# Optimization experiments

Measured on AMD Instinct MI355X. Metric: run time of the kernel, lower is better.

The kernel has to match this reference:

```python
import jax, jax.numpy as jnp
import numpy as np

DIM = 768
HEADS = 12
HEAD_DIM = DIM // HEADS
SCALE = HEAD_DIM ** -0.5
ALPHA = 0.1


def setup_inputs() -> dict:
    key = jax.random.key(0)
    ks = jax.random.split(key, 6)
    B, N, C = 16, 577, DIM
    x = jax.random.normal(ks[0], (B, N, C), dtype=jnp.float32)
    attn_weight = jax.random.uniform(ks[1], (B, N - 1), dtype=jnp.float32)
    w_qkv = jax.random.normal(ks[2], (C, 3 * C), dtype=jnp.float32) * (C ** -0.5)
    b_qkv = jnp.zeros((3 * C,), dtype=jnp.float32)
    w_proj = jax.random.normal(ks[3], (C, C), dtype=jnp.float32) * (C ** -0.5)
    b_proj = jnp.zeros((C,), dtype=jnp.float32)
    return {"x": x, "attn_weight": attn_weight, "w_qkv": w_qkv, "b_qkv": b_qkv,
            "w_proj": w_proj, "b_proj": b_proj}


def reference(x, attn_weight, w_qkv, b_qkv, w_proj, b_proj):
    B, N, C = x.shape
    H, D = HEADS, HEAD_DIM
    qkv = (x @ w_qkv + b_qkv).reshape(B, N, 3, H, D)
    qkv = jnp.transpose(qkv, (2, 0, 3, 1, 4))  # [3, B, H, N, D]
    q, k, v = qkv[0], qkv[1], qkv[2]
    attn = jnp.einsum('bhnd,bhmd->bhnm', q, k) * SCALE  # [B,H,N,N]
    patch_attn = attn[:, :, 0, 1:]  # pre-softmax CLS->patch scores
    # reweight CLS row (excluding CLS->CLS) before softmax
    w = attn_weight[:, None, None, :]  # [B,1,1,N-1]
    cls_row = attn[:, :, 0:1, 1:] * (w * ALPHA + (1.0 - ALPHA))
    attn = attn.at[:, :, 0:1, 1:].set(cls_row)
    attn = jax.nn.softmax(attn, axis=-1)
    out = jnp.einsum('bhnm,bhmd->bhnd', attn, v)
    out = jnp.transpose(out, (0, 2, 1, 3)).reshape(B, N, C)
    out = out @ w_proj + b_proj
    return out, patch_attn
```

## Files before the change

kernel.cpp:

```cpp
#include <hip/hip_runtime.h>
#include <hip/hip_bf16.h>
#include <math.h>

#define B_    16
#define N_    577
#define C_    768
#define H_    12
#define D_    64
#define M_    (B_ * N_)
#define MP_   9344
#define QKVN  2304
#define NP_   640
#define SCALE 0.125f
#define ALPHA 0.1f
#define OUT0  (B_ * N_ * C_)

#define NB_CONV 7008
#define NB_T1   1728
#define NB_T2   576

typedef __attribute__((ext_vector_type(8))) short short8;
typedef __attribute__((ext_vector_type(4))) float f32x4;
typedef __hip_bfloat16 bf16;

__device__ __forceinline__ float exp2fast(float x) {
    return __builtin_amdgcn_exp2f(x);
}

__device__ __forceinline__ void load16(const void* g, void* l) {
    __builtin_amdgcn_global_load_lds(
        (const __attribute__((address_space(1))) unsigned int*)g,
        (__attribute__((address_space(3))) unsigned int*)l, 16, 0, 0);
}

__device__ __forceinline__ f32x4 mfma16(short8 a, short8 b, f32x4 c) {
    return __builtin_amdgcn_mfma_f32_16x16x32_bf16(a, b, c, 0, 0, 0);
}

#define FENCE() asm volatile("" ::: "memory")
#define BARRIER() do { FENCE(); __builtin_amdgcn_s_barrier(); FENCE(); } while (0)

__global__ __launch_bounds__(256) void prep(const float* __restrict__ x,
                                            bf16* __restrict__ xb,
                                            const float* __restrict__ wq,
                                            bf16* __restrict__ wqT,
                                            const float* __restrict__ wp,
                                            bf16* __restrict__ wpT) {
    __shared__ float tile[32][33];
    const int bid = blockIdx.x;
    if (bid < NB_CONV) {
        int idx = bid * 256 + threadIdx.x;
        int m = idx / 192;
        bf16 tmp[4];
        if (m < M_) {
            float4 f = ((const float4*)x)[idx];
            tmp[0] = __float2bfloat16(f.x);
            tmp[1] = __float2bfloat16(f.y);
            tmp[2] = __float2bfloat16(f.z);
            tmp[3] = __float2bfloat16(f.w);
        } else {
            tmp[0] = tmp[1] = tmp[2] = tmp[3] = __float2bfloat16(0.f);
        }
        ((ushort4*)xb)[idx] = *(ushort4*)tmp;
        return;
    }
    const float* src; bf16* dst; int C, R, bx, by;
    if (bid < NB_CONV + NB_T1) {
        int r = bid - NB_CONV;
        bx = r % 72; by = r / 72; src = wq; dst = wqT; R = 768; C = QKVN;
    } else {
        int r = bid - NB_CONV - NB_T1;
        bx = r % 24; by = r / 24; src = wp; dst = wpT; R = 768; C = 768;
    }
    int cb = bx * 32, rb = by * 32;
    int tx = threadIdx.x & 31, ty = threadIdx.x >> 5;
    #pragma unroll
    for (int i = 0; i < 32; i += 8)
        tile[ty + i][tx] = src[(size_t)(rb + ty + i) * C + cb + tx];
    __syncthreads();
    #pragma unroll
    for (int i = 0; i < 32; i += 8)
        dst[(size_t)(cb + ty + i) * R + rb + tx] = __float2bfloat16(tile[tx][ty + i]);
}

__global__ __launch_bounds__(256, 4) void gemm128(const bf16* __restrict__ A,
                                                  const bf16* __restrict__ BT,
                                                  const float* __restrict__ bias,
                                                  bf16* __restrict__ q,
                                                  bf16* __restrict__ kk,
                                                  bf16* __restrict__ vt,
                                                  float* __restrict__ out,
                                                  int mode, int nby) {
    __shared__ __align__(16) char smem[35840];

    const int nwg = gridDim.x;
    const int orig = blockIdx.x;
    const int xcd = orig & 7, ii = orig >> 3;
    const int qq = nwg >> 3, rr = nwg & 7;
    const int wg = (xcd < rr ? xcd * (qq + 1) : rr * (qq + 1) + (xcd - rr) * qq) + ii;
    const int mb = wg / nby;
    const int nb = wg - mb * nby;
    const int m0 = mb * 128, n0 = nb * 128;
    const int t = threadIdx.x, lane = t & 63, w = t >> 6;
    const int wr = w >> 1, wc = w & 1;
    const int r16 = lane & 15, quad = lane >> 4;

    f32x4 acc[4][4];
    #pragma unroll
    for (int i = 0; i < 4; i++)
        #pragma unroll
        for (int j = 0; j < 4; j++) acc[i][j] = (f32x4)(0.f);

    const int lrow = lane >> 3;
    const int clog = ((lane & 7) ^ lrow) << 4;
    const char* gA = (const char*)A  + (size_t)(m0 + w * 32 + lrow) * 1536 + clog;
    const char* gB = (const char*)BT + (size_t)(n0 + w * 32 + lrow) * 1536 + clog;

    auto stage = [&](int k2) {
        const int kc = k2 * 128;
        #pragma unroll
        for (int i = 0; i < 4; i++) {
            char* dA = (char*)smem + w * 4096 + i * 1024;
            load16(gA + (size_t)i * 12288 + kc, dA);
            load16(gB + (size_t)i * 12288 + kc, dA + 16384);
        }
    };

    stage(0);
    asm volatile("s_waitcnt vmcnt(0)" ::: "memory");
    BARRIER();

    const int sw = r16 & 7;
    const int g0 = (quad ^ sw) << 4;
    const int g1 = ((quad ^ 4) ^ sw) << 4;

    #pragma unroll 1
    for (int k = 0; k < 12; k++) {
        const char* Ap = (const char*)smem + (wr * 64 + r16) * 128;
        const char* Bp = (const char*)smem + 16384 + (wc * 64 + r16) * 128;

        short8 a[4], b[4];
        #pragma unroll
        for (int mi = 0; mi < 4; mi++) a[mi] = *(const short8*)(Ap + mi * 2048 + g0);
        #pragma unroll
        for (int nj = 0; nj < 4; nj++) b[nj] = *(const short8*)(Bp + nj * 2048 + g0);
        __builtin_amdgcn_s_setprio(1);
        #pragma unroll
        for (int mi = 0; mi < 4; mi++)
            #pragma unroll
            for (int nj = 0; nj < 4; nj++)
                acc[mi][nj] = mfma16(a[mi], b[nj], acc[mi][nj]);
        __builtin_amdgcn_s_setprio(0);

        #pragma unroll
        for (int mi = 0; mi < 4; mi++) a[mi] = *(const short8*)(Ap + mi * 2048 + g1);
        #pragma unroll
        for (int nj = 0; nj < 4; nj++) b[nj] = *(const short8*)(Bp + nj * 2048 + g1);
        __builtin_amdgcn_s_setprio(1);
        #pragma unroll
        for (int mi = 0; mi < 4; mi++)
            #pragma unroll
            for (int nj = 0; nj < 4; nj++)
                acc[mi][nj] = mfma16(a[mi], b[nj], acc[mi][nj]);
        __builtin_amdgcn_s_setprio(0);

        BARRIER();
        if (k < 11) {
            stage(k + 1);
            asm volatile("s_waitcnt vmcnt(0)" ::: "memory");
            BARRIER();
        }
    }

    float bs[4];
    #pragma unroll
    for (int nj = 0; nj < 4; nj++) bs[nj] = bias[n0 + wc * 64 + nj * 16 + r16];

    if (mode == 1) {
        #pragma unroll
        for (int mi = 0; mi < 4; mi++) {
            #pragma unroll
            for (int nj = 0; nj < 4; nj++) {
                #pragma unroll
                for (int r = 0; r < 4; r++) {
                    int m = m0 + wr * 64 + mi * 16 + quad * 4 + r;
                    if (m >= M_) continue;
                    int cc = n0 + wc * 64 + nj * 16 + r16;
                    out[(size_t)m * 768 + cc] = acc[mi][nj][r] + bs[nj];
                }
            }
        }
        return;
    }

    bf16* Tt = (bf16*)smem;
    #pragma unroll
    for (int mi = 0; mi < 4; mi++) {
        #pragma unroll
        for (int nj = 0; nj < 4; nj++) {
            bf16 pk[4];
            #pragma unroll
            for (int r = 0; r < 4; r++)
                pk[r] = __float2bfloat16(acc[mi][nj][r] + bs[nj]);
            int ccl = wc * 64 + nj * 16 + r16;
            int ml4 = wr * 64 + mi * 16 + quad * 4;
            *(uint2*)&Tt[ccl * 140 + ml4] = *(const uint2*)pk;
        }
    }
    __syncthreads();

    const int part = nb / 6;
    if (part < 2) {
        int nl = t & 127, half = t >> 7;
        int m = m0 + nl;
        if (m < M_) {
            int b = m / N_, n = m - b * N_;
            int h = (nb % 6) * 2 + half;
            bf16* dst = (part == 0 ? q : kk) + ((size_t)(b * H_ + h) * N_ + n) * 64;
            #pragma unroll
            for (int d8 = 0; d8 < 8; d8++) {
                bf16 tv[8];
                #pragma unroll
                for (int dd = 0; dd < 8; dd++)
                    tv[dd] = Tt[(half * 64 + d8 * 8 + dd) * 140 + nl];
                *(uint4*)(dst + d8 * 8) = *(const uint4*)tv;
            }
        }
    } else {
        int dr = t >> 1, seg = t & 1;
        int rem = (nb % 6) * 128 + dr;
        int h = rem >> 6, d = rem & 63;
        int mb2 = m0 + seg * 64;
        int b = mb2 / N_;
        int n = mb2 - b * N_;
        const bf16* src = Tt + dr * 140 + seg * 64;
        int i = 0;
        while (i < 64 && mb2 + i < M_) {
            if (n == N_) { b++; n = 0; }
            bf16* drow = vt + ((size_t)(b * H_ + h) * 64 + d) * NP_;
            if ((n & 7) == 0 && n + 8 <= N_ && i + 8 <= 64 && mb2 + i + 8 <= M_) {
                bf16 tv[8];
                #pragma unroll
                for (int dd = 0; dd < 8; dd++) tv[dd] = src[i + dd];
                *(uint4*)(drow + n) = *(const uint4*)tv;
                i += 8; n += 8;
            } else {
                drow[n] = src[i]; i++; n++;
            }
        }
    }
}

__global__ __launch_bounds__(256) void attn_mfma(const bf16* __restrict__ q,
                                                 const bf16* __restrict__ k,
                                                 const bf16* __restrict__ vt,
                                                 const float* __restrict__ aw,
                                                 bf16* __restrict__ ao,
                                                 float* __restrict__ patch) {
    __shared__ bf16 Kb[2][4096];
    __shared__ bf16 Vb[2][4096];
    __shared__ bf16 Pb[4][2048];
    const int bh = blockIdx.x, qt = blockIdx.y;
    const int b = bh / H_, h = bh - b * H_;
    const int t = threadIdx.x, lane = t & 63, w = t >> 6;
    const int r16 = lane & 15, quad = lane >> 4;
    const float SC2 = SCALE * 1.44269504f;

    const bf16* kbp = k + (size_t)bh * N_ * 64;
    const bf16* vbp = vt + (size_t)bh * 64 * NP_;

    short8 qa0[2], qa1[2];
    #pragma unroll
    for (int mi = 0; mi < 2; mi++) {
        int qrow = qt * 128 + w * 32 + mi * 16 + r16;
        int qrc = (qrow < N_) ? qrow : (N_ - 1);
        const bf16* qp = q + ((size_t)bh * N_ + qrc) * 64 + quad * 8;
        qa0[mi] = *(const short8*)(qp);
        qa1[mi] = *(const short8*)(qp + 32);
    }

    f32x4 Oacc[2][4];
    #pragma unroll
    for (int mi = 0; mi < 2; mi++)
        #pragma unroll
        for (int d0 = 0; d0 < 4; d0++) Oacc[mi][d0] = (f32x4)(0.f);
    float lrow[2][4];
    #pragma unroll
    for (int mi = 0; mi < 2; mi++)
        #pragma unroll
        for (int rr = 0; rr < 4; rr++) lrow[mi][rr] = 0.f;

    const bool clsrow = (qt == 0) && (w == 0) && (quad == 0);

    auto stage = [&](int kt, int buf) {
        #pragma unroll
        for (int is = 0; is < 2; is++) {
            int base = is * 256 + w * 64;
            int slot = base + lane;
            int row = slot >> 3, pos = slot & 7;
            int c = pos ^ (row & 7);
            int jg = kt * 64 + row; if (jg > N_ - 1) jg = N_ - 1;
            load16(kbp + (size_t)jg * 64 + c * 8, &Kb[buf][base * 8]);
        }
        #pragma unroll
        for (int is = 0; is < 2; is++) {
            int base = is * 256 + w * 64;
            int slot = base + lane;
            int row = slot >> 3, pos = slot & 7;
            int c = pos ^ (row & 7);
            load16(vbp + (size_t)row * NP_ + kt * 64 + c * 8, &Vb[buf][base * 8]);
        }
    };

    stage(0, 0);
    __syncthreads();

    for (int kt = 0; kt < 10; kt++) {
        const int cur = kt & 1;
        if (kt < 9) stage(kt + 1, cur ^ 1);

        f32x4 S[2][4];
        #pragma unroll
        for (int j0 = 0; j0 < 4; j0++) {
            int row = j0 * 16 + r16;
            const bf16* kpl = &Kb[cur][row * 64];
            short8 kf0 = *(const short8*)(kpl + ((quad ^ (row & 7)) << 3));
            short8 kf1 = *(const short8*)(kpl + (((quad ^ 4) ^ (row & 7)) << 3));
            #pragma unroll
            for (int mi = 0; mi < 2; mi++) {
                f32x4 sa = (f32x4)(0.f);
                sa = mfma16(qa0[mi], kf0, sa);
                sa = mfma16(qa1[mi], kf1, sa);
                S[mi][j0] = sa;
            }
        }

        if (kt < 9) {
            #pragma unroll
            for (int mi = 0; mi < 2; mi++) {
                #pragma unroll
                for (int j0 = 0; j0 < 4; j0++) {
                    float wfac = 1.f;
                    if (mi == 0 && clsrow) {
                        int c = kt * 64 + j0 * 16 + r16;
                        if (c >= 1) {
                            patch[(size_t)bh * (N_ - 1) + (c - 1)] = S[0][j0][0] * SCALE;
                            wfac = aw[b * (N_ - 1) + (c - 1)] * ALPHA + (1.f - ALPHA);
                        }
                    }
                    #pragma unroll
                    for (int rr = 0; rr < 4; rr++) {
                        float v = S[mi][j0][rr] * SC2;
                        if (rr == 0) v *= wfac;
                        float p = exp2fast(v);
                        S[mi][j0][rr] = p;
                        lrow[mi][rr] += p;
                    }
                }
            }
        } else {
            #pragma unroll
            for (int mi = 0; mi < 2; mi++) {
                #pragma unroll
                for (int j0 = 0; j0 < 4; j0++) {
                    int c = kt * 64 + j0 * 16 + r16;
                    bool valid = (c < N_);
                    float wfac = 1.f;
                    if (mi == 0 && clsrow && valid) {
                        patch[(size_t)bh * (N_ - 1) + (c - 1)] = S[0][j0][0] * SCALE;
                        wfac = aw[b * (N_ - 1) + (c - 1)] * ALPHA + (1.f - ALPHA);
                    }
                    #pragma unroll
                    for (int rr = 0; rr < 4; rr++) {
                        float v = S[mi][j0][rr] * SC2;
                        if (rr == 0) v *= wfac;
                        float p = valid ? exp2fast(v) : 0.f;
                        S[mi][j0][rr] = p;
                        lrow[mi][rr] += p;
                    }
                }
            }
        }

        bf16* pw = &Pb[w][0];
        #pragma unroll
        for (int mi = 0; mi < 2; mi++) {
            #pragma unroll
            for (int j0 = 0; j0 < 4; j0++) {
                int cg = j0 * 2 + (r16 >> 3);
                #pragma unroll
                for (int rr = 0; rr < 4; rr++) {
                    int rp = mi * 16 + quad * 4 + rr;
                    pw[rp * 64 + ((cg ^ (rp & 7)) << 3) + (r16 & 7)] =
                        __float2bfloat16(S[mi][j0][rr]);
                }
            }
        }
        short8 pa0[2], pa1[2];
        #pragma unroll
        for (int mi = 0; mi < 2; mi++) {
            int rp = mi * 16 + r16;
            const bf16* pr = pw + rp * 64;
            pa0[mi] = *(const short8*)(pr + ((quad ^ (rp & 7)) << 3));
            pa1[mi] = *(const short8*)(pr + (((quad ^ 4) ^ (rp & 7)) << 3));
        }

        #pragma unroll
        for (int d0 = 0; d0 < 4; d0++) {
            int row = d0 * 16 + r16;
            const bf16* vpl = &Vb[cur][row * 64];
            short8 vf0 = *(const short8*)(vpl + ((quad ^ (row & 7)) << 3));
            short8 vf1 = *(const short8*)(vpl + (((quad ^ 4) ^ (row & 7)) << 3));
            #pragma unroll
            for (int mi = 0; mi < 2; mi++) {
                Oacc[mi][d0] = mfma16(pa0[mi], vf0, Oacc[mi][d0]);
                Oacc[mi][d0] = mfma16(pa1[mi], vf1, Oacc[mi][d0]);
            }
        }
        __syncthreads();
    }

    #pragma unroll
    for (int mi = 0; mi < 2; mi++) {
        #pragma unroll
        for (int rr = 0; rr < 4; rr++) {
            float l = lrow[mi][rr];
            l += __shfl_xor(l, 1);
            l += __shfl_xor(l, 2);
            l += __shfl_xor(l, 4);
            l += __shfl_xor(l, 8);
            int n = qt * 128 + w * 32 + mi * 16 + quad * 4 + rr;
            if (n >= N_) continue;
            float inv = 1.f / l;
            #pragma unroll
            for (int d0 = 0; d0 < 4; d0++) {
                ao[((size_t)(b * N_ + n) * H_ + h) * 64 + d0 * 16 + r16] =
                    __float2bfloat16(Oacc[mi][d0][rr] * inv);
            }
        }
    }
}

extern "C" void kernel_launch(void* const* d_in, const int* in_sizes, int n_in,
                              void* d_out, int out_size, void* d_ws, size_t ws_size,
                              hipStream_t stream) {
    const float* x      = (const float*)d_in[0];
    const float* aw     = (const float*)d_in[1];
    const float* w_qkv  = (const float*)d_in[2];
    const float* b_qkv  = (const float*)d_in[3];
    const float* w_proj = (const float*)d_in[4];
    const float* b_proj = (const float*)d_in[5];
    float* out = (float*)d_out;

    char* ws = (char*)d_ws;
    bf16* xbf    = (bf16*)(ws);
    bf16* wqkvT  = (bf16*)(ws + 14352384);
    bf16* wprojT = (bf16*)(ws + 17891328);
    bf16* qv     = (bf16*)(ws + 19070976);
    bf16* kv     = (bf16*)(ws + 33251328);
    bf16* vt     = (bf16*)(ws + 47431680);
    bf16* ao     = xbf;

    prep<<<NB_CONV + NB_T1 + NB_T2, 256, 0, stream>>>(x, xbf, w_qkv, wqkvT, w_proj, wprojT);

    gemm128<<<73 * 18, 256, 0, stream>>>(
        xbf, wqkvT, b_qkv, qv, kv, vt, nullptr, 0, 18);

    attn_mfma<<<dim3(H_ * B_, 5), 256, 0, stream>>>(qv, kv, vt, aw, ao, out + OUT0);

    gemm128<<<73 * 6, 256, 0, stream>>>(
        ao, wprojT, b_proj, nullptr, nullptr, nullptr, out, 1, 6);
}
```

Before: 216.8 us.

## Widen GEMM tiles to 128x256 with each wave owning a 64-column strip

The GEMM tile grows from 128x128 to 128x256. Each of the four waves now computes the full 128 rows against its own 64 columns, holding 8x4 accumulators, and the grid shrinks by half for both the QKV and projection launches. The goal is more reuse of each loaded A tile and fewer workgroups re-reading A from memory. The costs are higher register and LDS pressure (occupancy hint drops from 4 to 3) and fewer blocks: 219 for the projection GEMM, which may underfill 256 CUs. The scatter epilogue now runs in two phases because the LDS transpose buffer holds only 128 columns at a time.

```diff
diff --git a/kernel.cpp b/kernel.cpp
--- a/kernel.cpp
+++ b/kernel.cpp
@@ -83,15 +83,15 @@
         dst[(size_t)(cb + ty + i) * R + rb + tx] = __float2bfloat16(tile[tx][ty + i]);
 }
 
-__global__ __launch_bounds__(256, 4) void gemm128(const bf16* __restrict__ A,
-                                                  const bf16* __restrict__ BT,
-                                                  const float* __restrict__ bias,
-                                                  bf16* __restrict__ q,
-                                                  bf16* __restrict__ kk,
-                                                  bf16* __restrict__ vt,
-                                                  float* __restrict__ out,
-                                                  int mode, int nby) {
-    __shared__ __align__(16) char smem[35840];
+__global__ __launch_bounds__(256, 3) void gemmw(const bf16* __restrict__ A,
+                                                const bf16* __restrict__ BT,
+                                                const float* __restrict__ bias,
+                                                bf16* __restrict__ q,
+                                                bf16* __restrict__ kk,
+                                                bf16* __restrict__ vt,
+                                                float* __restrict__ out,
+                                                int mode, int nby) {
+    __shared__ __align__(16) char smem[49152];
 
     const int nwg = gridDim.x;
     const int orig = blockIdx.x;
@@ -100,29 +100,29 @@
     const int wg = (xcd < rr ? xcd * (qq + 1) : rr * (qq + 1) + (xcd - rr) * qq) + ii;
     const int mb = wg / nby;
     const int nb = wg - mb * nby;
-    const int m0 = mb * 128, n0 = nb * 128;
+    const int m0 = mb * 128, n0 = nb * 256;
     const int t = threadIdx.x, lane = t & 63, w = t >> 6;
-    const int wr = w >> 1, wc = w & 1;
     const int r16 = lane & 15, quad = lane >> 4;
 
-    f32x4 acc[4][4];
-    #pragma unroll
-    for (int i = 0; i < 4; i++)
+    f32x4 acc[8][4];
+    #pragma unroll
+    for (int i = 0; i < 8; i++)
         #pragma unroll
         for (int j = 0; j < 4; j++) acc[i][j] = (f32x4)(0.f);
 
     const int lrow = lane >> 3;
     const int clog = ((lane & 7) ^ lrow) << 4;
-    const char* gA = (const char*)A  + (size_t)(m0 + w * 32 + lrow) * 1536 + clog;
-    const char* gB = (const char*)BT + (size_t)(n0 + w * 32 + lrow) * 1536 + clog;
+    const char* gA = (const char*)A  + (size_t)(m0 + lrow) * 1536 + clog;
+    const char* gB = (const char*)BT + (size_t)(n0 + lrow) * 1536 + clog;
 
     auto stage = [&](int k2) {
         const int kc = k2 * 128;
         #pragma unroll
-        for (int i = 0; i < 4; i++) {
-            char* dA = (char*)smem + w * 4096 + i * 1024;
-            load16(gA + (size_t)i * 12288 + kc, dA);
-            load16(gB + (size_t)i * 12288 + kc, dA + 16384);
+        for (int i = 0; i < 12; i++) {
+            const int s = w * 12 + i;
+            const char* src = (s < 16) ? (gA + (size_t)s * 12288 + kc)
+                                       : (gB + (size_t)(s - 16) * 12288 + kc);
+            load16(src, (char*)smem + s * 1024);
         }
     };
 
@@ -134,34 +134,53 @@
     const int g0 = (quad ^ sw) << 4;
     const int g1 = ((quad ^ 4) ^ sw) << 4;
 
+    const char* Ap = (const char*)smem + r16 * 128;
+    const char* Bp = (const char*)smem + 16384 + (w * 64 + r16) * 128;
+
     #pragma unroll 1
     for (int k = 0; k < 12; k++) {
-        const char* Ap = (const char*)smem + (wr * 64 + r16) * 128;
-        const char* Bp = (const char*)smem + 16384 + (wc * 64 + r16) * 128;
-
-        short8 a[4], b[4];
-        #pragma unroll
-        for (int mi = 0; mi < 4; mi++) a[mi] = *(const short8*)(Ap + mi * 2048 + g0);
+        short8 a4[4], b[4];
+
         #pragma unroll
         for (int nj = 0; nj < 4; nj++) b[nj] = *(const short8*)(Bp + nj * 2048 + g0);
+        #pragma unroll
+        for (int mi = 0; mi < 4; mi++) a4[mi] = *(const short8*)(Ap + mi * 2048 + g0);
         __builtin_amdgcn_s_setprio(1);
         #pragma unroll
         for (int mi = 0; mi < 4; mi++)
             #pragma unroll
             for (int nj = 0; nj < 4; nj++)
-                acc[mi][nj] = mfma16(a[mi], b[nj], acc[mi][nj]);
+                acc[mi][nj] = mfma16(a4[mi], b[nj], acc[mi][nj]);
         __builtin_amdgcn_s_setprio(0);
-
-        #pragma unroll
-        for (int mi = 0; mi < 4; mi++) a[mi] = *(const short8*)(Ap + mi * 2048 + g1);
+        #pragma unroll
+        for (int mi = 0; mi < 4; mi++) a4[mi] = *(const short8*)(Ap + (mi + 4) * 2048 + g0);
+        __builtin_amdgcn_s_setprio(1);
+        #pragma unroll
+        for (int mi = 0; mi < 4; mi++)
+            #pragma unroll
+            for (int nj = 0; nj < 4; nj++)
+                acc[mi + 4][nj] = mfma16(a4[mi], b[nj], acc[mi + 4][nj]);
+        __builtin_amdgcn_s_setprio(0);
+
         #pragma unroll
         for (int nj = 0; nj < 4; nj++) b[nj] = *(const short8*)(Bp + nj * 2048 + g1);
+        #pragma unroll
+        for (int mi = 0; mi < 4; mi++) a4[mi] = *(const short8*)(Ap + mi * 2048 + g1);
         __builtin_amdgcn_s_setprio(1);
         #pragma unroll
         for (int mi = 0; mi < 4; mi++)
             #pragma unroll
             for (int nj = 0; nj < 4; nj++)
-                acc[mi][nj] = mfma16(a[mi], b[nj], acc[mi][nj]);
+                acc[mi][nj] = mfma16(a4[mi], b[nj], acc[mi][nj]);
+        __builtin_amdgcn_s_setprio(0);
+        #pragma unroll
+        for (int mi = 0; mi < 4; mi++) a4[mi] = *(const short8*)(Ap + (mi + 4) * 2048 + g1);
+        __builtin_amdgcn_s_setprio(1);
+        #pragma unroll
+        for (int mi = 0; mi < 4; mi++)
+            #pragma unroll
+            for (int nj = 0; nj < 4; nj++)
+                acc[mi + 4][nj] = mfma16(a4[mi], b[nj], acc[mi + 4][nj]);
         __builtin_amdgcn_s_setprio(0);
 
         BARRIER();
@@ -174,18 +193,18 @@
 
     float bs[4];
     #pragma unroll
-    for (int nj = 0; nj < 4; nj++) bs[nj] = bias[n0 + wc * 64 + nj * 16 + r16];
+    for (int nj = 0; nj < 4; nj++) bs[nj] = bias[n0 + w * 64 + nj * 16 + r16];
 
     if (mode == 1) {
         #pragma unroll
-        for (int mi = 0; mi < 4; mi++) {
+        for (int mi = 0; mi < 8; mi++) {
             #pragma unroll
             for (int nj = 0; nj < 4; nj++) {
                 #pragma unroll
                 for (int r = 0; r < 4; r++) {
-                    int m = m0 + wr * 64 + mi * 16 + quad * 4 + r;
+                    int m = m0 + mi * 16 + quad * 4 + r;
                     if (m >= M_) continue;
-                    int cc = n0 + wc * 64 + nj * 16 + r16;
+                    int cc = n0 + w * 64 + nj * 16 + r16;
                     out[(size_t)m * 768 + cc] = acc[mi][nj][r] + bs[nj];
                 }
             }
@@ -195,57 +214,63 @@
 
     bf16* Tt = (bf16*)smem;
     #pragma unroll
-    for (int mi = 0; mi < 4; mi++) {
-        #pragma unroll
-        for (int nj = 0; nj < 4; nj++) {
-            bf16 pk[4];
-            #pragma unroll
-            for (int r = 0; r < 4; r++)
-                pk[r] = __float2bfloat16(acc[mi][nj][r] + bs[nj]);
-            int ccl = wc * 64 + nj * 16 + r16;
-            int ml4 = wr * 64 + mi * 16 + quad * 4;
-            *(uint2*)&Tt[ccl * 140 + ml4] = *(const uint2*)pk;
-        }
-    }
-    __syncthreads();
-
-    const int part = nb / 6;
-    if (part < 2) {
-        int nl = t & 127, half = t >> 7;
-        int m = m0 + nl;
-        if (m < M_) {
-            int b = m / N_, n = m - b * N_;
-            int h = (nb % 6) * 2 + half;
-            bf16* dst = (part == 0 ? q : kk) + ((size_t)(b * H_ + h) * N_ + n) * 64;
-            #pragma unroll
-            for (int d8 = 0; d8 < 8; d8++) {
-                bf16 tv[8];
-                #pragma unroll
-                for (int dd = 0; dd < 8; dd++)
-                    tv[dd] = Tt[(half * 64 + d8 * 8 + dd) * 140 + nl];
-                *(uint4*)(dst + d8 * 8) = *(const uint4*)tv;
-            }
-        }
-    } else {
-        int dr = t >> 1, seg = t & 1;
-        int rem = (nb % 6) * 128 + dr;
-        int h = rem >> 6, d = rem & 63;
-        int mb2 = m0 + seg * 64;
-        int b = mb2 / N_;
-        int n = mb2 - b * N_;
-        const bf16* src = Tt + dr * 140 + seg * 64;
-        int i = 0;
-        while (i < 64 && mb2 + i < M_) {
-            if (n == N_) { b++; n = 0; }
-            bf16* drow = vt + ((size_t)(b * H_ + h) * 64 + d) * NP_;
-            if ((n & 7) == 0 && n + 8 <= N_ && i + 8 <= 64 && mb2 + i + 8 <= M_) {
-                bf16 tv[8];
-                #pragma unroll
-                for (int dd = 0; dd < 8; dd++) tv[dd] = src[i + dd];
-                *(uint4*)(drow + n) = *(const uint4*)tv;
-                i += 8; n += 8;
-            } else {
-                drow[n] = src[i]; i++; n++;
+    for (int ph = 0; ph < 2; ph++) {
+        __syncthreads();
+        if ((w >> 1) == ph) {
+            #pragma unroll
+            for (int mi = 0; mi < 8; mi++) {
+                #pragma unroll
+                for (int nj = 0; nj < 4; nj++) {
+                    bf16 pk[4];
+                    #pragma unroll
+                    for (int r = 0; r < 4; r++)
+                        pk[r] = __float2bfloat16(acc[mi][nj][r] + bs[nj]);
+                    int ccl = (w & 1) * 64 + nj * 16 + r16;
+                    int ml4 = mi * 16 + quad * 4;
+                    *(uint2*)&Tt[ccl * 140 + ml4] = *(const uint2*)pk;
+                }
+            }
+        }
+        __syncthreads();
+        const int cb2 = nb * 2 + ph;
+        const int part = cb2 / 6;
+        if (part < 2) {
+            int nl = t & 127, half = t >> 7;
+            int m = m0 + nl;
+            if (m < M_) {
+                int b = m / N_, n = m - b * N_;
+                int h = (cb2 % 6) * 2 + half;
+                bf16* dst = (part == 0 ? q : kk) + ((size_t)(b * H_ + h) * N_ + n) * 64;
+                #pragma unroll
+                for (int d8 = 0; d8 < 8; d8++) {
+                    bf16 tv[8];
+                    #pragma unroll
+                    for (int dd = 0; dd < 8; dd++)
+                        tv[dd] = Tt[(half * 64 + d8 * 8 + dd) * 140 + nl];
+                    *(uint4*)(dst + d8 * 8) = *(const uint4*)tv;
+                }
+            }
+        } else {
+            int dr = t >> 1, seg = t & 1;
+            int rem = (cb2 % 6) * 128 + dr;
+            int h = rem >> 6, d = rem & 63;
+            int mb2 = m0 + seg * 64;
+            int b = mb2 / N_;
+            int n = mb2 - b * N_;
+            const bf16* src = Tt + dr * 140 + seg * 64;
+            int i = 0;
+            while (i < 64 && mb2 + i < M_) {
+                if (n == N_) { b++; n = 0; }
+                bf16* drow = vt + ((size_t)(b * H_ + h) * 64 + d) * NP_;
+                if ((n & 7) == 0 && n + 8 <= N_ && i + 8 <= 64 && mb2 + i + 8 <= M_) {
+                    bf16 tv[8];
+                    #pragma unroll
+                    for (int dd = 0; dd < 8; dd++) tv[dd] = src[i + dd];
+                    *(uint4*)(drow + n) = *(const uint4*)tv;
+                    i += 8; n += 8;
+                } else {
+                    drow[n] = src[i]; i++; n++;
+                }
             }
         }
     }
@@ -463,11 +488,11 @@
 
     prep<<<NB_CONV + NB_T1 + NB_T2, 256, 0, stream>>>(x, xbf, w_qkv, wqkvT, w_proj, wprojT);
 
-    gemm128<<<73 * 18, 256, 0, stream>>>(
-        xbf, wqkvT, b_qkv, qv, kv, vt, nullptr, 0, 18);
+    gemmw<<<73 * 9, 256, 0, stream>>>(
+        xbf, wqkvT, b_qkv, qv, kv, vt, nullptr, 0, 9);
 
     attn_mfma<<<dim3(H_ * B_, 5), 256, 0, stream>>>(qv, kv, vt, aw, ao, out + OUT0);
 
-    gemm128<<<73 * 6, 256, 0, stream>>>(
-        ao, wprojT, b_proj, nullptr, nullptr, nullptr, out, 1, 6);
-}
+    gemmw<<<73 * 3, 256, 0, stream>>>(
+        ao, wprojT, b_proj, nullptr, nullptr, nullptr, out, 1, 3);
+}
```

New measurement: 277.9 us. 1.28x slower.
